# Performance work log

Hardware: AMD Instinct MI355X
Metric: run time of the kernel (lower is better)

## Reference

```python
import jax, jax.numpy as jnp
import numpy as np

B, T, E, H = 2, 2048, 1024, 16
HS = E // H  # head size 64


def setup_inputs() -> dict:
    key = jax.random.key(0)
    ks = jax.random.split(key, 6)
    s = 0.02
    return {
        "x": jax.random.normal(ks[0], (B, T, E), dtype=jnp.float32),
        "Wq": jax.random.normal(ks[1], (E, E), dtype=jnp.float32) * s,
        "Wk": jax.random.normal(ks[2], (E, E), dtype=jnp.float32) * s,
        "Wv": jax.random.normal(ks[3], (E, E), dtype=jnp.float32) * s,
        "Wp": jax.random.normal(ks[4], (E, E), dtype=jnp.float32) * s,
        "bp": jax.random.normal(ks[5], (E,), dtype=jnp.float32) * s,
    }


def reference(x, Wq, Wk, Wv, Wp, bp):
    b, t, e = x.shape
    # per-head projections (concatenated heads == single E->E matmul, reshaped)
    def heads(w):
        return jnp.einsum('bte,ef->btf', x, w).reshape(b, t, H, HS).transpose(0, 2, 1, 3)
    q, k, v = heads(Wq), heads(Wk), heads(Wv)  # [B,H,T,HS]
    # NOTE: original scales by full embed dim E, not head_size
    scores = jnp.einsum('bhqd,bhkd->bhqk', q, k) * (e ** -0.5)
    causal = jnp.tril(jnp.ones((t, t), dtype=bool))
    scores = jnp.where(causal, scores, -jnp.inf)
    probs = jax.nn.softmax(scores, axis=-1)
    # dropout is identity in eval mode
    out = jnp.einsum('bhqk,bhkd->bhqd', probs, v)  # [B,H,T,HS]
    out = out.transpose(0, 2, 1, 3).reshape(b, t, e)
    return jnp.einsum('bte,ef->btf', out, Wp) + bp
```

## Files before the change

kernel.cpp:

```cpp
#include <hip/hip_runtime.h>
#include <math.h>

typedef __bf16 bf16x8 __attribute__((ext_vector_type(8)));
typedef __bf16 bf16x4 __attribute__((ext_vector_type(4)));
typedef float f32x4 __attribute__((ext_vector_type(4)));

constexpr int Bb = 2, Tt = 2048, Ee = 1024, Hh = 16, Hs = 64;
constexpr int Mm = Bb * Tt;

__device__ inline unsigned short f2bf(float f) {
    union { float f; unsigned u; } c; c.f = f;
    unsigned u = c.u;
    u += 0x7FFFu + ((u >> 16) & 1u);
    return (unsigned short)(u >> 16);
}

#if __has_builtin(__builtin_amdgcn_exp2f)
#define EXP2(x) __builtin_amdgcn_exp2f(x)
#else
#define EXP2(x) exp2f(x)
#endif

__device__ inline void gl2lds16(const void* g, void* l) {
    __builtin_amdgcn_global_load_lds(
        (const __attribute__((address_space(1))) void*)g,
        (__attribute__((address_space(3))) void*)l, 16, 0, 0);
}

__device__ inline unsigned pk_bf16(float a, float b) {
    union { float f; unsigned u; } ca, cb;
    ca.f = a; cb.f = b;
    return __builtin_amdgcn_perm(ca.u + 0x8000u, cb.u + 0x8000u, 0x07060302u);
}

__global__ __launch_bounds__(256) void prep(const float* __restrict__ x,
                                            const float* __restrict__ Wq,
                                            const float* __restrict__ Wk,
                                            const float* __restrict__ Wv,
                                            const float* __restrict__ Wp,
                                            unsigned short* __restrict__ xb,
                                            unsigned short* __restrict__ wt3,
                                            unsigned short* __restrict__ wpt) {
    const int tid = threadIdx.x;
    if (blockIdx.z == 4) {
        int flat = (blockIdx.y * 16 + blockIdx.x) * 256 + tid;
#pragma unroll
        for (int i = 0; i < 16; i++) {
            int gid = flat + i * 65536;
            float4 v = ((const float4*)x)[gid];
            ushort4 o;
            o.x = f2bf(v.x); o.y = f2bf(v.y); o.z = f2bf(v.z); o.w = f2bf(v.w);
            ((ushort4*)xb)[gid] = o;
        }
        return;
    }
    __shared__ unsigned short t[64][68];
    const float* W = (blockIdx.z == 0) ? Wq : (blockIdx.z == 1) ? Wk
                    : (blockIdx.z == 2) ? Wv : Wp;
    unsigned short* dst = (blockIdx.z < 3) ? wt3 + (size_t)blockIdx.z * 1024 * 1024 : wpt;
    const int k0 = blockIdx.x * 64, n0 = blockIdx.y * 64;
#pragma unroll
    for (int j = 0; j < 4; j++) {
        int row = (tid >> 4) + j * 16;
        int c4 = (tid & 15) * 4;
        float4 v = *(const float4*)&W[(size_t)(k0 + row) * 1024 + n0 + c4];
        t[row][c4 + 0] = f2bf(v.x); t[row][c4 + 1] = f2bf(v.y);
        t[row][c4 + 2] = f2bf(v.z); t[row][c4 + 3] = f2bf(v.w);
    }
    __syncthreads();
#pragma unroll
    for (int j = 0; j < 16; j++) {
        int flat = j * 256 + tid;
        int orow = flat >> 6, ocol = flat & 63;
        dst[(size_t)(n0 + orow) * 1024 + k0 + ocol] = t[ocol][orow];
    }
}

__device__ inline void gemm_mainloop(const unsigned short* __restrict__ A,
                                     const unsigned short* __restrict__ Bt,
                                     unsigned short* As, unsigned short* Bs,
                                     int bm, int bn, int tid, f32x4 (&acc)[4][4]) {
    const int lane = tid & 63, w = tid >> 6;
    const int quad = lane >> 4, cl = lane & 15;
    const int wm = (w >> 1) * 64, wn = (w & 1) * 64;

    auto stage = [&](int k0) {
#pragma unroll
        for (int i = 0; i < 2; i++) {
            int L = tid + i * 256;
            int r = L >> 2;
            int kc = (L & 3) ^ (r & 3);
            gl2lds16(A + (size_t)(bm + r) * 1024 + k0 + kc * 8, &As[L * 8]);
        }
#pragma unroll
        for (int i = 0; i < 2; i++) {
            int L = tid + i * 256;
            int r = L >> 2;
            int kc = (L & 3) ^ (r & 3);
            gl2lds16(Bt + (size_t)(bn + r) * 1024 + k0 + kc * 8, &Bs[L * 8]);
        }
    };

    stage(0);
    __syncthreads();
    for (int k0 = 0;;) {
        bf16x8 af[4], bfr[4];
#pragma unroll
        for (int mt = 0; mt < 4; mt++) {
            int r = wm + mt * 16 + cl;
            af[mt] = *(const bf16x8*)&As[(r * 4 + (quad ^ (r & 3))) * 8];
            int rb = wn + mt * 16 + cl;
            bfr[mt] = *(const bf16x8*)&Bs[(rb * 4 + (quad ^ (rb & 3))) * 8];
        }
#pragma unroll
        for (int mt = 0; mt < 4; mt++)
#pragma unroll
            for (int nt = 0; nt < 4; nt++)
                acc[mt][nt] = __builtin_amdgcn_mfma_f32_16x16x32_bf16(
                    af[mt], bfr[nt], acc[mt][nt], 0, 0, 0);
        k0 += 32;
        if (k0 >= 1024) break;
        __syncthreads();
        stage(k0);
        __syncthreads();
    }
}

__global__ __launch_bounds__(256, 2) void gemm_qkv(const unsigned short* __restrict__ A,
                                                   const unsigned short* __restrict__ Bt,
                                                   unsigned short* __restrict__ qb,
                                                   unsigned short* __restrict__ kb,
                                                   unsigned short* __restrict__ vtb) {
    __shared__ unsigned short As[128 * 32];
    __shared__ unsigned short Bs[128 * 32];
    const int tid = threadIdx.x;
    const int bm = blockIdx.y * 128;
    const int bn = blockIdx.x * 128;
    f32x4 acc[4][4] = {};
    gemm_mainloop(A, Bt, As, Bs, bm, bn, tid, acc);

    const int lane = tid & 63, w = tid >> 6;
    const int quad = lane >> 4, cl = lane & 15;
    const int wm = (w >> 1) * 64, wn = (w & 1) * 64;
    const int region = bn >> 10;

    if (region < 2) {
        unsigned short* dst = region ? kb : qb;
        const float qs = region ? 1.0f : 0.045084220027780107f;
#pragma unroll
        for (int mt = 0; mt < 4; mt++)
#pragma unroll
            for (int nt = 0; nt < 4; nt++)
#pragma unroll
                for (int rg = 0; rg < 4; rg++) {
                    int m = bm + wm + mt * 16 + quad * 4 + rg;
                    int nn = (bn + wn + nt * 16 + cl) & 1023;
                    int b = m >> 11, t = m & 2047, h = nn >> 6, hs = nn & 63;
                    dst[((size_t)(b * 16 + h) * 2048 + t) * 64 + hs] =
                        f2bf(acc[mt][nt][rg] * qs);
                }
    } else {
#pragma unroll
        for (int mt = 0; mt < 4; mt++) {
            int m0 = bm + wm + mt * 16 + quad * 4;
            int b = m0 >> 11, t0 = m0 & 2047;
#pragma unroll
            for (int nt = 0; nt < 4; nt++) {
                int nn = (bn + wn + nt * 16 + cl) & 1023;
                int h = nn >> 6, hs = nn & 63;
                ushort4 pk;
                pk.x = f2bf(acc[mt][nt][0]); pk.y = f2bf(acc[mt][nt][1]);
                pk.z = f2bf(acc[mt][nt][2]); pk.w = f2bf(acc[mt][nt][3]);
                *(ushort4*)&vtb[((size_t)(b * 16 + h) * 64 + hs) * 2048 + t0] = pk;
            }
        }
    }
}

__global__ __launch_bounds__(256, 4) void gemm_out(const unsigned short* __restrict__ A,
                                                   const unsigned short* __restrict__ Bt,
                                                   const float* __restrict__ bias,
                                                   float* __restrict__ out) {
    __shared__ unsigned short As[64 * 32];
    __shared__ unsigned short Bs[128 * 32];
    const int tid = threadIdx.x;
    const int bm = blockIdx.y * 64;
    const int bn = blockIdx.x * 128;
    const int lane = tid & 63, w = tid >> 6;
    const int quad = lane >> 4, cl = lane & 15;
    const int wm = (w >> 1) * 32, wn = (w & 1) * 64;
    f32x4 acc[2][4] = {};

    auto stage = [&](int k0) {
        {
            int L = tid;
            int r = L >> 2;
            int kc = (L & 3) ^ (r & 3);
            gl2lds16(A + (size_t)(bm + r) * 1024 + k0 + kc * 8, &As[L * 8]);
        }
#pragma unroll
        for (int i = 0; i < 2; i++) {
            int L = tid + i * 256;
            int r = L >> 2;
            int kc = (L & 3) ^ (r & 3);
            gl2lds16(Bt + (size_t)(bn + r) * 1024 + k0 + kc * 8, &Bs[L * 8]);
        }
    };

    stage(0);
    __syncthreads();
    for (int k0 = 0;;) {
        bf16x8 af[2], bfr[4];
#pragma unroll
        for (int mt = 0; mt < 2; mt++) {
            int r = wm + mt * 16 + cl;
            af[mt] = *(const bf16x8*)&As[(r * 4 + (quad ^ (r & 3))) * 8];
        }
#pragma unroll
        for (int nt = 0; nt < 4; nt++) {
            int rb = wn + nt * 16 + cl;
            bfr[nt] = *(const bf16x8*)&Bs[(rb * 4 + (quad ^ (rb & 3))) * 8];
        }
#pragma unroll
        for (int mt = 0; mt < 2; mt++)
#pragma unroll
            for (int nt = 0; nt < 4; nt++)
                acc[mt][nt] = __builtin_amdgcn_mfma_f32_16x16x32_bf16(
                    af[mt], bfr[nt], acc[mt][nt], 0, 0, 0);
        k0 += 32;
        if (k0 >= 1024) break;
        __syncthreads();
        stage(k0);
        __syncthreads();
    }

#pragma unroll
    for (int mt = 0; mt < 2; mt++)
#pragma unroll
        for (int nt = 0; nt < 4; nt++)
#pragma unroll
            for (int rg = 0; rg < 4; rg++) {
                int m = bm + wm + mt * 16 + quad * 4 + rg;
                int n = bn + wn + nt * 16 + cl;
                out[(size_t)m * 1024 + n] = acc[mt][nt][rg] + bias[n];
            }
}

__global__ __launch_bounds__(512, 2) void attn_mfma(const unsigned short* __restrict__ qg,
                                                    const unsigned short* __restrict__ kg,
                                                    const unsigned short* __restrict__ vtg,
                                                    unsigned short* __restrict__ og) {
    __shared__ unsigned short lds[40960];
    float* Cmb = (float*)lds;
    float* Ll = (float*)(lds + 17408);

    const int tid = threadIdx.x;
    const int idx = blockIdx.x;
    const int bh = idx & 31;
    const int hi = idx >> 5;
    const int qt = (hi < 8) ? (15 - hi) : (hi - 8);
    const int lane = tid & 63, w = tid >> 6;
    const int quad = lane >> 4, cl = lane & 15;
    const int p = w >> 2;
    const int qq = w & 3;
    const int qbase = qt * 128;
    const int row_lo = qbase + qq * 32;
    const int kmax = 2 * qt + 1;
    const unsigned short* qB = qg + (size_t)bh * 2048 * 64;
    const unsigned short* kB = kg + (size_t)bh * 2048 * 64;
    const unsigned short* vB = vtg + (size_t)bh * 64 * 2048;

    auto stageKV = [&](int kt) {
        unsigned short* Kd = lds + (kt & 3) * 4096;
        unsigned short* Vd = lds + 16384 + (kt & 3) * 4096;
        int L = tid;
        int r = L >> 3;
        int kc = (L & 7) ^ (r & 7);
        gl2lds16(kB + (size_t)(kt * 64 + r) * 64 + kc * 8, &Kd[L * 8]);
        gl2lds16(vB + (size_t)r * 2048 + kt * 64 + kc * 8, &Vd[L * 8]);
    };

    bf16x8 qf[2][2];
#pragma unroll
    for (int nt2 = 0; nt2 < 2; nt2++)
#pragma unroll
        for (int kf = 0; kf < 2; kf++) {
            int row = row_lo + nt2 * 16 + cl;
            qf[nt2][kf] = *(const bf16x8*)&qB[(size_t)row * 64 + (kf * 4 + quad) * 8];
        }

    bf16x8 ones;
#pragma unroll
    for (int i = 0; i < 8; i++) ones[i] = (__bf16)1.0f;

    f32x4 oacc[2][4] = {};
    f32x4 lacc[2] = {};
    unsigned short* Pw = lds + 32768 + w * 1024;
    const int nit = qt + 1;

    stageKV(0);
    stageKV(1);
    __syncthreads();

    for (int i = 0; i < nit; i++) {
        if (2 * i + 2 <= kmax) stageKV(2 * i + 2);
        if (2 * i + 3 <= kmax) stageKV(2 * i + 3);

        const int kt = 2 * i + p;
        if (kt * 64 <= row_lo + 31) {
            const bool diag = (kt * 64 + 63 > row_lo);
            const int d0 = row_lo - kt * 64;
            const unsigned short* Kl = lds + (kt & 3) * 4096;
            const unsigned short* Vl = lds + 16384 + (kt & 3) * 4096;
            f32x4 sac[4][2] = {};
#pragma unroll
            for (int kf = 0; kf < 2; kf++)
#pragma unroll
                for (int mt = 0; mt < 4; mt++) {
                    int r = mt * 16 + cl, cc = kf * 4 + quad;
                    bf16x8 kf8 = *(const bf16x8*)&Kl[(r * 8 + (cc ^ (r & 7))) * 8];
#pragma unroll
                    for (int nt2 = 0; nt2 < 2; nt2++)
                        sac[mt][nt2] = __builtin_amdgcn_mfma_f32_16x16x32_bf16(
                            kf8, qf[nt2][kf], sac[mt][nt2], 0, 0, 0);
                }
#pragma unroll
            for (int ks = 0; ks < 2; ks++) {
#pragma unroll
                for (int mtl = 0; mtl < 2; mtl++)
#pragma unroll
                    for (int nt2 = 0; nt2 < 2; nt2++) {
                        float pv[4];
#pragma unroll
                        for (int rg = 0; rg < 4; rg++) {
                            float e = EXP2(sac[ks * 2 + mtl][nt2][rg]);
                            if (diag && (ks * 32 + mtl * 16 + quad * 4 + rg >
                                         d0 + nt2 * 16 + cl))
                                e = 0.0f;
                            pv[rg] = e;
                        }
                        uint2 d;
                        d.x = pk_bf16(pv[1], pv[0]);
                        d.y = pk_bf16(pv[3], pv[2]);
                        int r2 = nt2 * 16 + cl;
                        int c = mtl * 2 + (quad >> 1);
                        int pc = c ^ ((r2 >> 1) & 3);
                        *(uint2*)&Pw[r2 * 32 + pc * 8 + (quad & 1) * 4] = d;
                    }
                bf16x8 pf[2];
#pragma unroll
                for (int mt2 = 0; mt2 < 2; mt2++) {
                    int r2 = mt2 * 16 + cl;
                    int pc = quad ^ ((r2 >> 1) & 3);
                    pf[mt2] = *(const bf16x8*)&Pw[r2 * 32 + pc * 8];
                }
#pragma unroll
                for (int mt2 = 0; mt2 < 2; mt2++)
                    lacc[mt2] = __builtin_amdgcn_mfma_f32_16x16x32_bf16(
                        pf[mt2], ones, lacc[mt2], 0, 0, 0);
#pragma unroll
                for (int nt = 0; nt < 4; nt++) {
                    int r = nt * 16 + cl, cc = ks * 4 + quad;
                    bf16x8 vf = *(const bf16x8*)&Vl[(r * 8 + (cc ^ (r & 7))) * 8];
#pragma unroll
                    for (int mt2 = 0; mt2 < 2; mt2++)
                        oacc[mt2][nt] = __builtin_amdgcn_mfma_f32_16x16x32_bf16(
                            pf[mt2], vf, oacc[mt2][nt], 0, 0, 0);
                }
            }
        }
        __syncthreads();
    }

    if (p == 1) {
#pragma unroll
        for (int mt2 = 0; mt2 < 2; mt2++)
#pragma unroll
            for (int rg = 0; rg < 4; rg++) {
                int row = qq * 32 + mt2 * 16 + quad * 4 + rg;
                if (cl == 0) Ll[row] = lacc[mt2][rg];
#pragma unroll
                for (int nt = 0; nt < 4; nt++)
                    Cmb[row * 68 + nt * 16 + cl] = oacc[mt2][nt][rg];
            }
    }
    __syncthreads();
    if (p == 0) {
        const int b = bh >> 4, h = bh & 15;
#pragma unroll
        for (int mt2 = 0; mt2 < 2; mt2++)
#pragma unroll
            for (int rg = 0; rg < 4; rg++) {
                int row = qq * 32 + mt2 * 16 + quad * 4 + rg;
                float inv = 1.0f / (lacc[mt2][rg] + Ll[row]);
                int t = qbase + row;
#pragma unroll
                for (int nt = 0; nt < 4; nt++) {
                    int hs = nt * 16 + cl;
                    float val = oacc[mt2][nt][rg] + Cmb[row * 68 + nt * 16 + cl];
                    og[((size_t)(b * 2048 + t)) * 1024 + h * 64 + hs] = f2bf(val * inv);
                }
            }
    }
}

extern "C" void kernel_launch(void* const* d_in, const int* in_sizes, int n_in,
                              void* d_out, int out_size, void* d_ws, size_t ws_size,
                              hipStream_t stream) {
    const float* x = (const float*)d_in[0];
    const float* Wq = (const float*)d_in[1];
    const float* Wk = (const float*)d_in[2];
    const float* Wv = (const float*)d_in[3];
    const float* Wp = (const float*)d_in[4];
    const float* bp = (const float*)d_in[5];
    float* out = (float*)d_out;

    unsigned short* xb = (unsigned short*)d_ws;
    unsigned short* wt3 = xb + (size_t)Mm * Ee;
    unsigned short* wpt = wt3 + (size_t)3 * Ee * Ee;
    unsigned short* qb = wpt + (size_t)Ee * Ee;
    unsigned short* kb = qb + (size_t)Mm * Ee;
    unsigned short* vtb = kb + (size_t)Mm * Ee;
    unsigned short* ab = vtb + (size_t)Mm * Ee;

    prep<<<dim3(16, 16, 5), dim3(256), 0, stream>>>(x, Wq, Wk, Wv, Wp, xb, wt3, wpt);
    gemm_qkv<<<dim3(24, 32), dim3(256), 0, stream>>>(xb, wt3, qb, kb, vtb);
    attn_mfma<<<dim3(512), dim3(512), 0, stream>>>(qb, kb, vtb, ab);
    gemm_out<<<dim3(8, 64), dim3(256), 0, stream>>>(ab, wpt, bp, out);
}
```

Before: 176.8 us.

## Keep softmax probabilities in registers via permuted K row staging

K rows are loaded into LDS in a permuted order, so the S=K·Q^T MFMA output layout lines up directly with the A-operand layout needed for the P·V MFMA. The probabilities are packed into bf16x8 fragments in registers instead of being written to LDS and read back. This removes the per-wave P scratch area, shrinking LDS enough to raise the launch-bounds occupancy target from 2 to 4 blocks. It also adds s_setprio around the MFMA sections. The causal mask index is rewritten to match the new row permutation; a mistake there would break correctness.

New measurement: 181.2 us. 2.5% more time.

```diff
diff --git a/kernel.cpp b/kernel.cpp
--- a/kernel.cpp
+++ b/kernel.cpp
@@ -246,11 +246,11 @@
             }
 }
 
-__global__ __launch_bounds__(512, 2) void attn_mfma(const unsigned short* __restrict__ qg,
+__global__ __launch_bounds__(512, 4) void attn_mfma(const unsigned short* __restrict__ qg,
                                                     const unsigned short* __restrict__ kg,
                                                     const unsigned short* __restrict__ vtg,
                                                     unsigned short* __restrict__ og) {
-    __shared__ unsigned short lds[40960];
+    __shared__ unsigned short lds[32768];
     float* Cmb = (float*)lds;
     float* Ll = (float*)(lds + 17408);
 
@@ -276,7 +276,8 @@
         int L = tid;
         int r = L >> 3;
         int kc = (L & 7) ^ (r & 7);
-        gl2lds16(kB + (size_t)(kt * 64 + r) * 64 + kc * 8, &Kd[L * 8]);
+        int grow = (r & 32) | ((r & 12) << 1) | ((r & 16) >> 2) | (r & 3);
+        gl2lds16(kB + (size_t)(kt * 64 + grow) * 64 + kc * 8, &Kd[L * 8]);
         gl2lds16(vB + (size_t)r * 2048 + kt * 64 + kc * 8, &Vd[L * 8]);
     };
 
@@ -295,7 +296,6 @@
 
     f32x4 oacc[2][4] = {};
     f32x4 lacc[2] = {};
-    unsigned short* Pw = lds + 32768 + w * 1024;
     const int nit = qt + 1;
 
     stageKV(0);
@@ -313,6 +313,7 @@
             const unsigned short* Kl = lds + (kt & 3) * 4096;
             const unsigned short* Vl = lds + 16384 + (kt & 3) * 4096;
             f32x4 sac[4][2] = {};
+            __builtin_amdgcn_s_setprio(1);
 #pragma unroll
             for (int kf = 0; kf < 2; kf++)
 #pragma unroll
@@ -324,36 +325,32 @@
                         sac[mt][nt2] = __builtin_amdgcn_mfma_f32_16x16x32_bf16(
                             kf8, qf[nt2][kf], sac[mt][nt2], 0, 0, 0);
                 }
+            __builtin_amdgcn_s_setprio(0);
 #pragma unroll
             for (int ks = 0; ks < 2; ks++) {
-#pragma unroll
-                for (int mtl = 0; mtl < 2; mtl++)
-#pragma unroll
-                    for (int nt2 = 0; nt2 < 2; nt2++) {
+                bf16x8 pf[2];
+#pragma unroll
+                for (int nt2 = 0; nt2 < 2; nt2++) {
+                    unsigned dw[4];
+#pragma unroll
+                    for (int mtl = 0; mtl < 2; mtl++) {
                         float pv[4];
 #pragma unroll
                         for (int rg = 0; rg < 4; rg++) {
                             float e = EXP2(sac[ks * 2 + mtl][nt2][rg]);
-                            if (diag && (ks * 32 + mtl * 16 + quad * 4 + rg >
+                            if (diag && (ks * 32 + quad * 8 + mtl * 4 + rg >
                                          d0 + nt2 * 16 + cl))
                                 e = 0.0f;
                             pv[rg] = e;
                         }
-                        uint2 d;
-                        d.x = pk_bf16(pv[1], pv[0]);
-                        d.y = pk_bf16(pv[3], pv[2]);
-                        int r2 = nt2 * 16 + cl;
-                        int c = mtl * 2 + (quad >> 1);
-                        int pc = c ^ ((r2 >> 1) & 3);
-                        *(uint2*)&Pw[r2 * 32 + pc * 8 + (quad & 1) * 4] = d;
+                        dw[mtl * 2 + 0] = pk_bf16(pv[1], pv[0]);
+                        dw[mtl * 2 + 1] = pk_bf16(pv[3], pv[2]);
                     }
-                bf16x8 pf[2];
-#pragma unroll
-                for (int mt2 = 0; mt2 < 2; mt2++) {
-                    int r2 = mt2 * 16 + cl;
-                    int pc = quad ^ ((r2 >> 1) & 3);
-                    pf[mt2] = *(const bf16x8*)&Pw[r2 * 32 + pc * 8];
+                    union { uint4 u; bf16x8 v; } cv;
+                    cv.u = make_uint4(dw[0], dw[1], dw[2], dw[3]);
+                    pf[nt2] = cv.v;
                 }
+                __builtin_amdgcn_s_setprio(1);
 #pragma unroll
                 for (int mt2 = 0; mt2 < 2; mt2++)
                     lacc[mt2] = __builtin_amdgcn_mfma_f32_16x16x32_bf16(
@@ -367,6 +364,7 @@
                         oacc[mt2][nt] = __builtin_amdgcn_mfma_f32_16x16x32_bf16(
                             pf[mt2], vf, oacc[mt2][nt], 0, 0, 0);
                 }
+                __builtin_amdgcn_s_setprio(0);
             }
         }
         __syncthreads();
```
